# Kernel tuning notes

Hardware: AMD Instinct MI355X
Metric: run time of the kernel (lower is better)

Reference implementation:

```python
import jax, jax.numpy as jnp
import numpy as np

N = 100000

def gcn_conv(x, edge_index, W, b, num_nodes):
    # PyG GCNConv: add self-loops, symmetric deg^{-1/2} normalization, then linear.
    xw = x @ W  # [N, out]
    loops = jnp.arange(num_nodes, dtype=edge_index.dtype)
    src = jnp.concatenate([edge_index[0], loops])
    dst = jnp.concatenate([edge_index[1], loops])
    deg = jax.ops.segment_sum(jnp.ones_like(src, dtype=xw.dtype), dst, num_segments=num_nodes)
    dinv = jnp.where(deg > 0, jax.lax.rsqrt(deg), 0.0)
    norm = dinv[src] * dinv[dst]            # [E+N]
    msg = xw[src] * norm[:, None]           # gather + scale
    out = jax.ops.segment_sum(msg, dst, num_segments=num_nodes)  # scatter-add
    return out + b


def setup_inputs() -> dict:
    key = jax.random.key(0)
    ks = jax.random.split(key, 12)
    in_feat, hid, out_c = 64, 64, 16
    E = 1000000
    x = jax.random.normal(ks[0], (N, in_feat), dtype=jnp.float32)
    ei_spatial = jax.random.randint(ks[1], (2, E), 0, N, dtype=jnp.int32)
    ei_sim = jax.random.randint(ks[2], (2, E), 0, N, dtype=jnp.int32)
    def glorot(k, fi, fo):
        s = jnp.sqrt(6.0 / (fi + fo))
        return jax.random.uniform(k, (fi, fo), jnp.float32, -s, s)
    return {
        "x": x, "ei_spatial": ei_spatial, "ei_sim": ei_sim,
        "W1a": glorot(ks[3], in_feat, hid), "b1a": jnp.zeros((hid,), jnp.float32),
        "W1b": glorot(ks[4], in_feat, hid), "b1b": jnp.zeros((hid,), jnp.float32),
        "W2a": glorot(ks[5], hid, out_c), "b2a": jnp.zeros((out_c,), jnp.float32),
        "W2b": glorot(ks[6], hid, out_c), "b2b": jnp.zeros((out_c,), jnp.float32),
    }


def reference(x, ei_spatial, ei_sim, W1a, b1a, W1b, b1b, W2a, b2a, W2b, b2b):
    # HeteroConv layer 1: mean over the two relation-specific GCNConvs
    h = 0.5 * (gcn_conv(x, ei_spatial, W1a, b1a, N) + gcn_conv(x, ei_sim, W1b, b1b, N))
    h = jax.nn.relu(h)
    # HeteroConv layer 2
    out = 0.5 * (gcn_conv(h, ei_spatial, W2a, b2a, N) + gcn_conv(h, ei_sim, W2b, b2b, N))
    return out
```

## Files before the change

kernel.cpp:

```cpp
#include <hip/hip_runtime.h>

#define XS_STRIDE 72
#define MAXBUK 256
#define BF_CHUNK 4096

typedef unsigned short ushort_t;
typedef unsigned int uint_t;
typedef __attribute__((ext_vector_type(8))) short short8_t;
typedef __attribute__((ext_vector_type(4))) float f32x4;

__device__ __forceinline__ ushort_t f2bf(float x) {
    uint_t u = __float_as_uint(x);
    uint_t r = (u + 0x7FFFu + ((u >> 16) & 1u)) >> 16;
    return (ushort_t)r;
}
__device__ __forceinline__ float bf2f(ushort_t h) {
    return __uint_as_float((uint_t)h << 16);
}
__device__ __forceinline__ float bf2f_lo(uint_t g) { return __uint_as_float(g << 16); }
__device__ __forceinline__ float bf2f_hi(uint_t g) { return __uint_as_float(g & 0xFFFF0000u); }

__global__ void init_caps_kernel(int* bcursor2, int nbuk2, int CAP) {
    int i = blockIdx.x * blockDim.x + threadIdx.x;
    if (i < nbuk2) bcursor2[i] = i * CAP;
}

__global__ void bfill2_kernel(const int* __restrict__ eia, const int* __restrict__ eib,
                              int* __restrict__ bcursor, uint_t* __restrict__ pairs,
                              int Ea, int Eb, int Et, int shift, int nbuk, int n) {
    __shared__ int cnt[MAXBUK];
    __shared__ int base[MAXBUK];
    __shared__ int off[MAXBUK];
    const int t = threadIdx.x;
    const long long e0 = (long long)blockIdx.x * BF_CHUNK;
    const int nedge = (int)min((long long)BF_CHUNK, (long long)Et - e0);
    const int nbuk2 = 2 * nbuk;
    const uint_t mask = (1u << shift) - 1u;
    for (int i = t; i < nbuk2; i += 256) cnt[i] = 0;
    __syncthreads();
    for (int i = t; i < nedge; i += 256) {
        long long e = e0 + i;
        int rel = (e >= Ea);
        int d = rel ? eib[Eb + (e - Ea)] : eia[Ea + e];
        atomicAdd(&cnt[(rel ? nbuk : 0) + (d >> shift)], 1);
    }
    __syncthreads();
    for (int i = t; i < nbuk2; i += 256) {
        off[i] = 0;
        base[i] = cnt[i] ? atomicAdd(&bcursor[i], cnt[i]) : 0;
    }
    __syncthreads();
    for (int i = t; i < nedge; i += 256) {
        long long e = e0 + i;
        int rel = (e >= Ea);
        int s, d;
        if (rel) { s = eib[e - Ea]; d = eib[Eb + (e - Ea)]; }
        else     { s = eia[e];      d = eia[Ea + e]; }
        int b = (rel ? nbuk : 0) + (d >> shift);
        int p = base[b] + atomicAdd(&off[b], 1);
        pairs[p] = ((uint_t)s << shift) | ((uint_t)d & mask);
    }
}

template<int NPB>
__global__ void bucket_csr_kernel(const uint_t* __restrict__ pairs,
                                  const int* __restrict__ bcursor2,
                                  int2* __restrict__ rowse2, float* __restrict__ dinv2,
                                  int* __restrict__ col2,
                                  int nbuk, int shift, int n, int CAP) {
    constexpr int BLK = 1024;
    constexpr int K = NPB / BLK;
    constexpr uint_t MASK = NPB - 1;
    __shared__ int cnt[NPB];
    __shared__ int wsum[16];
    const int b = blockIdx.x;
    const int t = threadIdx.x;
    const int lane = t & 63;
    const int w = t >> 6;
    const int rel = (b >= nbuk);
    const int blocal = rel ? b - nbuk : b;
    const int nodelo = blocal << shift;
    const int node0 = (rel ? n : 0) + nodelo;
    const int NN = min(NPB, n - nodelo);
    const int p0 = b * CAP;
    const int p1 = bcursor2[b];

    #pragma unroll
    for (int k = 0; k < K; ++k) cnt[t + k * BLK] = 0;
    __syncthreads();
    for (int idx = p0 + t; idx < p1; idx += BLK)
        atomicAdd(&cnt[pairs[idx] & MASK], 1);
    __syncthreads();

    int a[K]; int s = 0;
    #pragma unroll
    for (int k = 0; k < K; ++k) { a[k] = cnt[t * K + k]; s += a[k]; }
    int sc = s;
    #pragma unroll
    for (int d = 1; d < 64; d <<= 1) {
        int u = __shfl_up(sc, d);
        if (lane >= d) sc += u;
    }
    if (lane == 63) wsum[w] = sc;
    __syncthreads();
    if (t < 16) {
        int v = wsum[t];
        int scc = v;
        #pragma unroll
        for (int d = 1; d < 16; d <<= 1) {
            int u = __shfl_up(scc, d);
            if (t >= d) scc += u;
        }
        wsum[t] = scc - v;
    }
    __syncthreads();
    int run = p0 + wsum[w] + sc - s;
    __syncthreads();
    #pragma unroll
    for (int k = 0; k < K; ++k) {
        int j = t * K + k;
        cnt[j] = run;
        if (j < NN) {
            rowse2[node0 + j] = make_int2(run, run + a[k]);
            dinv2[node0 + j] = rsqrtf((float)(a[k] + 1));
        }
        run += a[k];
    }
    __syncthreads();
    for (int idx = p0 + t; idx < p1; idx += BLK) {
        uint_t p = pairs[idx];
        int pos = atomicAdd(&cnt[p & MASK], 1);
        col2[pos] = (int)(p >> shift);
    }
}

__global__ void gemm2_mfma_bf16_kernel(const float* __restrict__ X,
                                       const float* __restrict__ Wa, const float* __restrict__ Wb,
                                       const float* __restrict__ dinva, const float* __restrict__ dinvb,
                                       ushort_t* __restrict__ ya, ushort_t* __restrict__ yb, int n) {
    __shared__ ushort_t Xs[64 * XS_STRIDE];
    __shared__ ushort_t Wt[128 * XS_STRIDE];
    const int tid = threadIdx.x;
    const int rowbase = blockIdx.x * 64;

    {
        int row = tid >> 2, cg = tid & 3;
        int grow = rowbase + row;
        float4 v[4];
        if (grow < n) {
            const float4* xr = reinterpret_cast<const float4*>(X + (size_t)grow * 64 + cg * 16);
            v[0] = xr[0]; v[1] = xr[1]; v[2] = xr[2]; v[3] = xr[3];
        } else {
            v[0] = v[1] = v[2] = v[3] = make_float4(0.f, 0.f, 0.f, 0.f);
        }
        ushort_t* dst = &Xs[row * XS_STRIDE + cg * 16];
        #pragma unroll
        for (int q = 0; q < 4; ++q) {
            dst[q * 4 + 0] = f2bf(v[q].x); dst[q * 4 + 1] = f2bf(v[q].y);
            dst[q * 4 + 2] = f2bf(v[q].z); dst[q * 4 + 3] = f2bf(v[q].w);
        }
    }
    for (int idx = tid; idx < 4096; idx += 256) {
        int k = idx >> 6, c = idx & 63;
        Wt[c * XS_STRIDE + k] = f2bf(Wa[idx]);
        Wt[(64 + c) * XS_STRIDE + k] = f2bf(Wb[idx]);
    }
    __syncthreads();

    const int wid = tid >> 6, lane = tid & 63;
    const int lrow = lane & 15;
    const int lk = (lane >> 4) * 8;

    short8_t a0 = *reinterpret_cast<const short8_t*>(&Xs[(wid * 16 + lrow) * XS_STRIDE + lk]);
    short8_t a1 = *reinterpret_cast<const short8_t*>(&Xs[(wid * 16 + lrow) * XS_STRIDE + 32 + lk]);

    f32x4 acc[8];
    #pragma unroll
    for (int ct = 0; ct < 8; ++ct) {
        short8_t b0 = *reinterpret_cast<const short8_t*>(&Wt[(ct * 16 + lrow) * XS_STRIDE + lk]);
        short8_t b1 = *reinterpret_cast<const short8_t*>(&Wt[(ct * 16 + lrow) * XS_STRIDE + 32 + lk]);
        f32x4 c = {0.f, 0.f, 0.f, 0.f};
        c = __builtin_amdgcn_mfma_f32_16x16x32_bf16(a0, b0, c, 0, 0, 0);
        c = __builtin_amdgcn_mfma_f32_16x16x32_bf16(a1, b1, c, 0, 0, 0);
        acc[ct] = c;
    }

    const int rq = (lane >> 4) * 4;
    #pragma unroll
    for (int r = 0; r < 4; ++r) {
        int grow = rowbase + wid * 16 + rq + r;
        if (grow < n) {
            float sa = dinva[grow], sb = dinvb[grow];
            #pragma unroll
            for (int ct = 0; ct < 8; ++ct) {
                int col = ct * 16 + lrow;
                float v = acc[ct][r];
                if (col < 64) ya[(size_t)grow * 64 + col] = f2bf(v * sa);
                else          yb[(size_t)grow * 64 + (col - 64)] = f2bf(v * sb);
            }
        }
    }
}

__global__ void gemm2_mfma_h_kernel(const ushort_t* __restrict__ H,
                                    const float* __restrict__ W2a, const float* __restrict__ W2b,
                                    const float* __restrict__ dinva, const float* __restrict__ dinvb,
                                    ushort_t* __restrict__ za, ushort_t* __restrict__ zb, int n) {
    __shared__ ushort_t Hs[64 * XS_STRIDE];
    __shared__ ushort_t Wt[32 * XS_STRIDE];
    const int tid = threadIdx.x;
    const int rowbase = blockIdx.x * 64;

    {
        int row = tid >> 2, cg = tid & 3;
        int grow = rowbase + row;
        uint4 v0 = {0, 0, 0, 0}, v1 = {0, 0, 0, 0};
        if (grow < n) {
            const uint4* hr = reinterpret_cast<const uint4*>(H + (size_t)grow * 64 + cg * 16);
            v0 = hr[0]; v1 = hr[1];
        }
        uint4* dst = reinterpret_cast<uint4*>(&Hs[row * XS_STRIDE + cg * 16]);
        dst[0] = v0; dst[1] = v1;
    }
    for (int idx = tid; idx < 2048; idx += 256) {
        int c = idx & 31, k = idx >> 5;
        float v = (c < 16) ? W2a[k * 16 + c] : W2b[k * 16 + (c - 16)];
        Wt[c * XS_STRIDE + k] = f2bf(v);
    }
    __syncthreads();

    const int wid = tid >> 6, lane = tid & 63;
    const int lrow = lane & 15;
    const int lk = (lane >> 4) * 8;
    const int rq = (lane >> 4) * 4;

    short8_t a0 = *reinterpret_cast<const short8_t*>(&Hs[(wid * 16 + lrow) * XS_STRIDE + lk]);
    short8_t a1 = *reinterpret_cast<const short8_t*>(&Hs[(wid * 16 + lrow) * XS_STRIDE + 32 + lk]);

    f32x4 c0 = {0.f, 0.f, 0.f, 0.f}, c1 = {0.f, 0.f, 0.f, 0.f};
    {
        short8_t b0 = *reinterpret_cast<const short8_t*>(&Wt[lrow * XS_STRIDE + lk]);
        short8_t b1 = *reinterpret_cast<const short8_t*>(&Wt[lrow * XS_STRIDE + 32 + lk]);
        c0 = __builtin_amdgcn_mfma_f32_16x16x32_bf16(a0, b0, c0, 0, 0, 0);
        c0 = __builtin_amdgcn_mfma_f32_16x16x32_bf16(a1, b1, c0, 0, 0, 0);
    }
    {
        short8_t b0 = *reinterpret_cast<const short8_t*>(&Wt[(16 + lrow) * XS_STRIDE + lk]);
        short8_t b1 = *reinterpret_cast<const short8_t*>(&Wt[(16 + lrow) * XS_STRIDE + 32 + lk]);
        c1 = __builtin_amdgcn_mfma_f32_16x16x32_bf16(a0, b0, c1, 0, 0, 0);
        c1 = __builtin_amdgcn_mfma_f32_16x16x32_bf16(a1, b1, c1, 0, 0, 0);
    }
    #pragma unroll
    for (int r = 0; r < 4; ++r) {
        int node = rowbase + wid * 16 + rq + r;
        if (node < n) {
            za[(size_t)node * 16 + lrow] = f2bf(c0[r] * dinva[node]);
            zb[(size_t)node * 16 + lrow] = f2bf(c1[r] * dinvb[node]);
        }
    }
}

__global__ void __launch_bounds__(256, 8)
agg64_dual_kernel(const ushort_t* __restrict__ ya, const ushort_t* __restrict__ yb,
                  const int2* __restrict__ rowse2, const int* __restrict__ col2,
                  const float* __restrict__ dinv2,
                  const float* __restrict__ ba, const float* __restrict__ bb,
                  ushort_t* __restrict__ h, int n) {
    const int lane = threadIdx.x & 63;
    const int half = lane >> 5;
    const int fp   = lane & 31;
    const int gw   = (blockIdx.x * blockDim.x + threadIdx.x) >> 6;
    const int nw   = (gridDim.x * blockDim.x) >> 6;
    const float bx = ba[2 * fp] + bb[2 * fp];
    const float by = ba[2 * fp + 1] + bb[2 * fp + 1];
    for (int i = gw; i < n; i += nw) {
        const int2 sea = rowse2[i];
        const int2 seb = rowse2[n + i];
        float ax = 0.f, ay = 0.f, bx2 = 0.f, by2 = 0.f;
        if (half == 0) {
            uint_t ga = *reinterpret_cast<const uint_t*>(ya + (size_t)i * 64 + 2 * fp);
            uint_t gb = *reinterpret_cast<const uint_t*>(yb + (size_t)i * 64 + 2 * fp);
            ax = bf2f_lo(ga); ay = bf2f_hi(ga);
            bx2 = bf2f_lo(gb); by2 = bf2f_hi(gb);
        }
        for (int base0 = sea.x; base0 < sea.y; base0 += 64) {
            const int m = min(64, sea.y - base0);
            int cv = (lane < m) ? col2[base0 + lane] : 0;
            int j = 0;
            for (; j + 8 <= m; j += 8) {
                int c0 = __shfl(cv, j + half),     c1 = __shfl(cv, j + 2 + half);
                int c2 = __shfl(cv, j + 4 + half), c3 = __shfl(cv, j + 6 + half);
                uint_t g0 = *reinterpret_cast<const uint_t*>(ya + (size_t)c0 * 64 + 2 * fp);
                uint_t g1 = *reinterpret_cast<const uint_t*>(ya + (size_t)c1 * 64 + 2 * fp);
                uint_t g2 = *reinterpret_cast<const uint_t*>(ya + (size_t)c2 * 64 + 2 * fp);
                uint_t g3 = *reinterpret_cast<const uint_t*>(ya + (size_t)c3 * 64 + 2 * fp);
                ax += (bf2f_lo(g0) + bf2f_lo(g1)) + (bf2f_lo(g2) + bf2f_lo(g3));
                ay += (bf2f_hi(g0) + bf2f_hi(g1)) + (bf2f_hi(g2) + bf2f_hi(g3));
            }
            for (; j + 2 <= m; j += 2) {
                int c = __shfl(cv, j + half);
                uint_t g = *reinterpret_cast<const uint_t*>(ya + (size_t)c * 64 + 2 * fp);
                ax += bf2f_lo(g); ay += bf2f_hi(g);
            }
            if (j < m) {
                int c = __shfl(cv, j);
                if (half == 0) {
                    uint_t g = *reinterpret_cast<const uint_t*>(ya + (size_t)c * 64 + 2 * fp);
                    ax += bf2f_lo(g); ay += bf2f_hi(g);
                }
            }
        }
        for (int base0 = seb.x; base0 < seb.y; base0 += 64) {
            const int m = min(64, seb.y - base0);
            int cv = (lane < m) ? col2[base0 + lane] : 0;
            int j = 0;
            for (; j + 8 <= m; j += 8) {
                int c0 = __shfl(cv, j + half),     c1 = __shfl(cv, j + 2 + half);
                int c2 = __shfl(cv, j + 4 + half), c3 = __shfl(cv, j + 6 + half);
                uint_t g0 = *reinterpret_cast<const uint_t*>(yb + (size_t)c0 * 64 + 2 * fp);
                uint_t g1 = *reinterpret_cast<const uint_t*>(yb + (size_t)c1 * 64 + 2 * fp);
                uint_t g2 = *reinterpret_cast<const uint_t*>(yb + (size_t)c2 * 64 + 2 * fp);
                uint_t g3 = *reinterpret_cast<const uint_t*>(yb + (size_t)c3 * 64 + 2 * fp);
                bx2 += (bf2f_lo(g0) + bf2f_lo(g1)) + (bf2f_lo(g2) + bf2f_lo(g3));
                by2 += (bf2f_hi(g0) + bf2f_hi(g1)) + (bf2f_hi(g2) + bf2f_hi(g3));
            }
            for (; j + 2 <= m; j += 2) {
                int c = __shfl(cv, j + half);
                uint_t g = *reinterpret_cast<const uint_t*>(yb + (size_t)c * 64 + 2 * fp);
                bx2 += bf2f_lo(g); by2 += bf2f_hi(g);
            }
            if (j < m) {
                int c = __shfl(cv, j);
                if (half == 0) {
                    uint_t g = *reinterpret_cast<const uint_t*>(yb + (size_t)c * 64 + 2 * fp);
                    bx2 += bf2f_lo(g); by2 += bf2f_hi(g);
                }
            }
        }
        ax += __shfl_xor(ax, 32);  ay += __shfl_xor(ay, 32);
        bx2 += __shfl_xor(bx2, 32); by2 += __shfl_xor(by2, 32);
        const float da = dinv2[i], db = dinv2[n + i];
        if (half == 0) {
            float vx = fmaxf(0.5f * (ax * da + bx2 * db + bx), 0.0f);
            float vy = fmaxf(0.5f * (ay * da + by2 * db + by), 0.0f);
            uint_t p = (uint_t)f2bf(vx) | ((uint_t)f2bf(vy) << 16);
            *reinterpret_cast<uint_t*>(h + (size_t)i * 64 + 2 * fp) = p;
        }
    }
}

__global__ void __launch_bounds__(256, 8)
agg16_dual_kernel(const ushort_t* __restrict__ za, const ushort_t* __restrict__ zb,
                  const int2* __restrict__ rowse2, const int* __restrict__ col2,
                  const float* __restrict__ dinv2,
                  const float* __restrict__ ba, const float* __restrict__ bb,
                  float* __restrict__ outp, int n) {
    const int lane = threadIdx.x & 63;
    const int fp   = lane & 7;
    const int sub  = lane >> 3;
    const int gw   = (blockIdx.x * blockDim.x + threadIdx.x) >> 6;
    const int nw   = (gridDim.x * blockDim.x) >> 6;
    const float bx = ba[2 * fp] + bb[2 * fp];
    const float by = ba[2 * fp + 1] + bb[2 * fp + 1];
    for (int i = gw; i < n; i += nw) {
        const int2 sea = rowse2[i];
        const int2 seb = rowse2[n + i];
        int ea = sea.x + sub, eb = seb.x + sub;
        const int e1a = sea.y, e1b = seb.y;
        float ax = 0.f, ay = 0.f, bx2 = 0.f, by2 = 0.f;
        if (sub == 0) {
            uint_t ga = *reinterpret_cast<const uint_t*>(za + (size_t)i * 16 + 2 * fp);
            uint_t gb = *reinterpret_cast<const uint_t*>(zb + (size_t)i * 16 + 2 * fp);
            ax = bf2f_lo(ga); ay = bf2f_hi(ga);
            bx2 = bf2f_lo(gb); by2 = bf2f_hi(gb);
        }
        for (; ea + 8 < e1a && eb + 8 < e1b; ea += 16, eb += 16) {
            int c0 = col2[ea], c1 = col2[ea + 8];
            int d0 = col2[eb], d1 = col2[eb + 8];
            uint_t g0 = *reinterpret_cast<const uint_t*>(za + (size_t)c0 * 16 + 2 * fp);
            uint_t g1 = *reinterpret_cast<const uint_t*>(za + (size_t)c1 * 16 + 2 * fp);
            uint_t g2 = *reinterpret_cast<const uint_t*>(zb + (size_t)d0 * 16 + 2 * fp);
            uint_t g3 = *reinterpret_cast<const uint_t*>(zb + (size_t)d1 * 16 + 2 * fp);
            ax += bf2f_lo(g0) + bf2f_lo(g1);  ay += bf2f_hi(g0) + bf2f_hi(g1);
            bx2 += bf2f_lo(g2) + bf2f_lo(g3); by2 += bf2f_hi(g2) + bf2f_hi(g3);
        }
        for (; ea < e1a; ea += 8) {
            uint_t g = *reinterpret_cast<const uint_t*>(za + (size_t)col2[ea] * 16 + 2 * fp);
            ax += bf2f_lo(g); ay += bf2f_hi(g);
        }
        for (; eb < e1b; eb += 8) {
            uint_t g = *reinterpret_cast<const uint_t*>(zb + (size_t)col2[eb] * 16 + 2 * fp);
            bx2 += bf2f_lo(g); by2 += bf2f_hi(g);
        }
        const float da = dinv2[i], db = dinv2[n + i];
        float vx = ax * da + bx2 * db;
        float vy = ay * da + by2 * db;
        vx += __shfl_xor(vx, 8);  vy += __shfl_xor(vy, 8);
        vx += __shfl_xor(vx, 16); vy += __shfl_xor(vy, 16);
        vx += __shfl_xor(vx, 32); vy += __shfl_xor(vy, 32);
        if (sub == 0) {
            float2 o = make_float2(0.5f * (vx + bx), 0.5f * (vy + by));
            *reinterpret_cast<float2*>(outp + (size_t)i * 16 + 2 * fp) = o;
        }
    }
}

extern "C" void kernel_launch(void* const* d_in, const int* in_sizes, int n_in,
                              void* d_out, int out_size, void* d_ws, size_t ws_size,
                              hipStream_t stream) {
    const float* x   = (const float*)d_in[0];
    const int*   eia = (const int*)d_in[1];
    const int*   eib = (const int*)d_in[2];
    const float* W1a = (const float*)d_in[3];
    const float* b1a = (const float*)d_in[4];
    const float* W1b = (const float*)d_in[5];
    const float* b1b = (const float*)d_in[6];
    const float* W2a = (const float*)d_in[7];
    const float* b2a = (const float*)d_in[8];
    const float* W2b = (const float*)d_in[9];
    const float* b2b = (const float*)d_in[10];
    float* out = (float*)d_out;

    const int n  = in_sizes[0] / 64;
    const int Ea = in_sizes[1] / 2;
    const int Eb = in_sizes[2] / 2;
    const int Et = Ea + Eb;
    const int n2 = 2 * n;

    int shift = 10;
    while ((((long long)n + (1LL << shift) - 1) >> shift) > 128) ++shift;
    const int nbuk = (int)(((long long)n + (1LL << shift) - 1) >> shift);
    const int nbuk2 = 2 * nbuk;
    const int Emaxrel = Ea > Eb ? Ea : Eb;
    int CAP = ((Emaxrel / (nbuk > 0 ? nbuk : 1)) * 3) / 2 + 2048;
    CAP = (CAP + 63) & ~63;

    char* wsp = (char*)d_ws;
    size_t off = 0;
    auto carve = [&](size_t elems) { void* p = wsp + off; off += ((elems + 3) & ~(size_t)3) * 4; return p; };
    float* dinv2    = (float*)carve(n2);
    int2*  rowse2   = (int2*)carve((size_t)n2 * 2);
    int*   bcursor2 = (int*)carve(MAXBUK);
    int*   col2     = (int*)carve((size_t)nbuk2 * CAP);
    ushort_t* ya    = (ushort_t*)carve((size_t)32 * n);
    ushort_t* yb    = (ushort_t*)carve((size_t)32 * n);
    ushort_t* za    = (ushort_t*)carve((size_t)8 * n);
    ushort_t* zb    = (ushort_t*)carve((size_t)8 * n);
    size_t pair_words = (size_t)nbuk2 * CAP;
    size_t big_words = pair_words > (size_t)32 * n ? pair_words : (size_t)32 * n;
    void*  big      = carve(big_words);
    uint_t* pairs   = (uint_t*)big;
    ushort_t* H     = (ushort_t*)big;

    const int T = 256;
    auto cdiv = [](long long a, long long b) { return (unsigned)((a + b - 1) / b); };

    init_caps_kernel<<<1, 256, 0, stream>>>(bcursor2, nbuk2, CAP);
    bfill2_kernel<<<cdiv(Et, BF_CHUNK), T, 0, stream>>>(eia, eib, bcursor2, pairs,
                                                        Ea, Eb, Et, shift, nbuk, n);
    if (shift == 10)
        bucket_csr_kernel<1024><<<nbuk2, 1024, 0, stream>>>(pairs, bcursor2, rowse2, dinv2,
                                                            col2, nbuk, shift, n, CAP);
    else if (shift == 11)
        bucket_csr_kernel<2048><<<nbuk2, 1024, 0, stream>>>(pairs, bcursor2, rowse2, dinv2,
                                                            col2, nbuk, shift, n, CAP);
    else
        bucket_csr_kernel<4096><<<nbuk2, 1024, 0, stream>>>(pairs, bcursor2, rowse2, dinv2,
                                                            col2, nbuk, shift, n, CAP);

    const unsigned AGG_GRID = 2048;

    gemm2_mfma_bf16_kernel<<<cdiv(n, 64), T, 0, stream>>>(x, W1a, W1b, dinv2, dinv2 + n, ya, yb, n);
    agg64_dual_kernel<<<AGG_GRID, T, 0, stream>>>(ya, yb, rowse2, col2, dinv2, b1a, b1b, H, n);

    gemm2_mfma_h_kernel<<<cdiv(n, 64), T, 0, stream>>>(H, W2a, W2b, dinv2, dinv2 + n, za, zb, n);
    agg16_dual_kernel<<<AGG_GRID, T, 0, stream>>>(za, zb, rowse2, col2, dinv2, b2a, b2b, out, n);
}
```

Before: 168.2 us.

## Interleave per-node CSR ranges and dinv, widen agg64 gathers to 8 bytes

Row start/end pairs for both relations are now packed as one int4 per node, and the two dinv values as one float2, so each consumer kernel does a single vector load instead of two scattered loads. The 64-feature aggregation kernel is also restructured so each lane gathers 4 bf16 features (8 bytes) while the wave handles 4 edges at once, instead of 2 features across 2 half-waves. The aim is fewer load instructions and better memory coalescing. The cost is an extra cross-lane reduction stage and more accumulator registers.

```diff
diff --git a/kernel.cpp b/kernel.cpp
--- a/kernel.cpp
+++ b/kernel.cpp
@@ -65,7 +65,7 @@
 template<int NPB>
 __global__ void bucket_csr_kernel(const uint_t* __restrict__ pairs,
                                   const int* __restrict__ bcursor2,
-                                  int2* __restrict__ rowse2, float* __restrict__ dinv2,
+                                  int* __restrict__ rowse, float* __restrict__ dinv,
                                   int* __restrict__ col2,
                                   int nbuk, int shift, int n, int CAP) {
     constexpr int BLK = 1024;
@@ -80,7 +80,6 @@
     const int rel = (b >= nbuk);
     const int blocal = rel ? b - nbuk : b;
     const int nodelo = blocal << shift;
-    const int node0 = (rel ? n : 0) + nodelo;
     const int NN = min(NPB, n - nodelo);
     const int p0 = b * CAP;
     const int p1 = bcursor2[b];
@@ -121,8 +120,10 @@
         int j = t * K + k;
         cnt[j] = run;
         if (j < NN) {
-            rowse2[node0 + j] = make_int2(run, run + a[k]);
-            dinv2[node0 + j] = rsqrtf((float)(a[k] + 1));
+            int node = nodelo + j;
+            *reinterpret_cast<int2*>(rowse + 4 * (size_t)node + (rel ? 2 : 0)) =
+                make_int2(run, run + a[k]);
+            dinv[2 * (size_t)node + rel] = rsqrtf((float)(a[k] + 1));
         }
         run += a[k];
     }
@@ -136,7 +137,7 @@
 
 __global__ void gemm2_mfma_bf16_kernel(const float* __restrict__ X,
                                        const float* __restrict__ Wa, const float* __restrict__ Wb,
-                                       const float* __restrict__ dinva, const float* __restrict__ dinvb,
+                                       const float2* __restrict__ dinv,
                                        ushort_t* __restrict__ ya, ushort_t* __restrict__ yb, int n) {
     __shared__ ushort_t Xs[64 * XS_STRIDE];
     __shared__ ushort_t Wt[128 * XS_STRIDE];
@@ -190,13 +191,13 @@
     for (int r = 0; r < 4; ++r) {
         int grow = rowbase + wid * 16 + rq + r;
         if (grow < n) {
-            float sa = dinva[grow], sb = dinvb[grow];
+            float2 dv = dinv[grow];
             #pragma unroll
             for (int ct = 0; ct < 8; ++ct) {
                 int col = ct * 16 + lrow;
                 float v = acc[ct][r];
-                if (col < 64) ya[(size_t)grow * 64 + col] = f2bf(v * sa);
-                else          yb[(size_t)grow * 64 + (col - 64)] = f2bf(v * sb);
+                if (col < 64) ya[(size_t)grow * 64 + col] = f2bf(v * dv.x);
+                else          yb[(size_t)grow * 64 + (col - 64)] = f2bf(v * dv.y);
             }
         }
     }
@@ -204,7 +205,7 @@
 
 __global__ void gemm2_mfma_h_kernel(const ushort_t* __restrict__ H,
                                     const float* __restrict__ W2a, const float* __restrict__ W2b,
-                                    const float* __restrict__ dinva, const float* __restrict__ dinvb,
+                                    const float2* __restrict__ dinv,
                                     ushort_t* __restrict__ za, ushort_t* __restrict__ zb, int n) {
     __shared__ ushort_t Hs[64 * XS_STRIDE];
     __shared__ ushort_t Wt[32 * XS_STRIDE];
@@ -254,105 +255,124 @@
     for (int r = 0; r < 4; ++r) {
         int node = rowbase + wid * 16 + rq + r;
         if (node < n) {
-            za[(size_t)node * 16 + lrow] = f2bf(c0[r] * dinva[node]);
-            zb[(size_t)node * 16 + lrow] = f2bf(c1[r] * dinvb[node]);
+            float2 dv = dinv[node];
+            za[(size_t)node * 16 + lrow] = f2bf(c0[r] * dv.x);
+            zb[(size_t)node * 16 + lrow] = f2bf(c1[r] * dv.y);
         }
     }
 }
 
 __global__ void __launch_bounds__(256, 8)
 agg64_dual_kernel(const ushort_t* __restrict__ ya, const ushort_t* __restrict__ yb,
-                  const int2* __restrict__ rowse2, const int* __restrict__ col2,
-                  const float* __restrict__ dinv2,
+                  const int4* __restrict__ rowse4, const int* __restrict__ col2,
+                  const float2* __restrict__ dinv,
                   const float* __restrict__ ba, const float* __restrict__ bb,
                   ushort_t* __restrict__ h, int n) {
     const int lane = threadIdx.x & 63;
-    const int half = lane >> 5;
-    const int fp   = lane & 31;
-    const int gw   = (blockIdx.x * blockDim.x + threadIdx.x) >> 6;
-    const int nw   = (gridDim.x * blockDim.x) >> 6;
-    const float bx = ba[2 * fp] + bb[2 * fp];
-    const float by = ba[2 * fp + 1] + bb[2 * fp + 1];
+    const int quarter = lane >> 4;
+    const int fp = lane & 15;
+    const int gw = (blockIdx.x * blockDim.x + threadIdx.x) >> 6;
+    const int nw = (gridDim.x * blockDim.x) >> 6;
+    const float bi0 = ba[4 * fp] + bb[4 * fp];
+    const float bi1 = ba[4 * fp + 1] + bb[4 * fp + 1];
+    const float bi2 = ba[4 * fp + 2] + bb[4 * fp + 2];
+    const float bi3 = ba[4 * fp + 3] + bb[4 * fp + 3];
     for (int i = gw; i < n; i += nw) {
-        const int2 sea = rowse2[i];
-        const int2 seb = rowse2[n + i];
-        float ax = 0.f, ay = 0.f, bx2 = 0.f, by2 = 0.f;
-        if (half == 0) {
-            uint_t ga = *reinterpret_cast<const uint_t*>(ya + (size_t)i * 64 + 2 * fp);
-            uint_t gb = *reinterpret_cast<const uint_t*>(yb + (size_t)i * 64 + 2 * fp);
-            ax = bf2f_lo(ga); ay = bf2f_hi(ga);
-            bx2 = bf2f_lo(gb); by2 = bf2f_hi(gb);
-        }
-        for (int base0 = sea.x; base0 < sea.y; base0 += 64) {
-            const int m = min(64, sea.y - base0);
+        const int4 se = rowse4[i];
+        const float2 dv = dinv[i];
+        float a0 = 0.f, a1 = 0.f, a2 = 0.f, a3 = 0.f;
+        float c0 = 0.f, c1 = 0.f, c2 = 0.f, c3 = 0.f;
+        if (quarter == 0) {
+            uint2 g = *reinterpret_cast<const uint2*>(ya + (size_t)i * 64 + 4 * fp);
+            a0 = bf2f_lo(g.x); a1 = bf2f_hi(g.x); a2 = bf2f_lo(g.y); a3 = bf2f_hi(g.y);
+            uint2 gb = *reinterpret_cast<const uint2*>(yb + (size_t)i * 64 + 4 * fp);
+            c0 = bf2f_lo(gb.x); c1 = bf2f_hi(gb.x); c2 = bf2f_lo(gb.y); c3 = bf2f_hi(gb.y);
+        }
+        for (int base0 = se.x; base0 < se.y; base0 += 64) {
+            const int m = min(64, se.y - base0);
             int cv = (lane < m) ? col2[base0 + lane] : 0;
             int j = 0;
             for (; j + 8 <= m; j += 8) {
-                int c0 = __shfl(cv, j + half),     c1 = __shfl(cv, j + 2 + half);
-                int c2 = __shfl(cv, j + 4 + half), c3 = __shfl(cv, j + 6 + half);
-                uint_t g0 = *reinterpret_cast<const uint_t*>(ya + (size_t)c0 * 64 + 2 * fp);
-                uint_t g1 = *reinterpret_cast<const uint_t*>(ya + (size_t)c1 * 64 + 2 * fp);
-                uint_t g2 = *reinterpret_cast<const uint_t*>(ya + (size_t)c2 * 64 + 2 * fp);
-                uint_t g3 = *reinterpret_cast<const uint_t*>(ya + (size_t)c3 * 64 + 2 * fp);
-                ax += (bf2f_lo(g0) + bf2f_lo(g1)) + (bf2f_lo(g2) + bf2f_lo(g3));
-                ay += (bf2f_hi(g0) + bf2f_hi(g1)) + (bf2f_hi(g2) + bf2f_hi(g3));
-            }
-            for (; j + 2 <= m; j += 2) {
-                int c = __shfl(cv, j + half);
-                uint_t g = *reinterpret_cast<const uint_t*>(ya + (size_t)c * 64 + 2 * fp);
-                ax += bf2f_lo(g); ay += bf2f_hi(g);
+                int e0 = __shfl(cv, j + quarter);
+                int e1 = __shfl(cv, j + 4 + quarter);
+                uint2 g0 = *reinterpret_cast<const uint2*>(ya + (size_t)e0 * 64 + 4 * fp);
+                uint2 g1 = *reinterpret_cast<const uint2*>(ya + (size_t)e1 * 64 + 4 * fp);
+                a0 += bf2f_lo(g0.x) + bf2f_lo(g1.x);
+                a1 += bf2f_hi(g0.x) + bf2f_hi(g1.x);
+                a2 += bf2f_lo(g0.y) + bf2f_lo(g1.y);
+                a3 += bf2f_hi(g0.y) + bf2f_hi(g1.y);
             }
             if (j < m) {
-                int c = __shfl(cv, j);
-                if (half == 0) {
-                    uint_t g = *reinterpret_cast<const uint_t*>(ya + (size_t)c * 64 + 2 * fp);
-                    ax += bf2f_lo(g); ay += bf2f_hi(g);
+                int i0 = j + quarter, i1 = j + 4 + quarter;
+                int e0 = __shfl(cv, i0 & 63);
+                int e1 = __shfl(cv, i1 & 63);
+                if (i0 < m) {
+                    uint2 g = *reinterpret_cast<const uint2*>(ya + (size_t)e0 * 64 + 4 * fp);
+                    a0 += bf2f_lo(g.x); a1 += bf2f_hi(g.x);
+                    a2 += bf2f_lo(g.y); a3 += bf2f_hi(g.y);
+                }
+                if (i1 < m) {
+                    uint2 g = *reinterpret_cast<const uint2*>(ya + (size_t)e1 * 64 + 4 * fp);
+                    a0 += bf2f_lo(g.x); a1 += bf2f_hi(g.x);
+                    a2 += bf2f_lo(g.y); a3 += bf2f_hi(g.y);
                 }
             }
         }
-        for (int base0 = seb.x; base0 < seb.y; base0 += 64) {
-            const int m = min(64, seb.y - base0);
+        for (int base0 = se.z; base0 < se.w; base0 += 64) {
+            const int m = min(64, se.w - base0);
             int cv = (lane < m) ? col2[base0 + lane] : 0;
             int j = 0;
             for (; j + 8 <= m; j += 8) {
-                int c0 = __shfl(cv, j + half),     c1 = __shfl(cv, j + 2 + half);
-                int c2 = __shfl(cv, j + 4 + half), c3 = __shfl(cv, j + 6 + half);
-                uint_t g0 = *reinterpret_cast<const uint_t*>(yb + (size_t)c0 * 64 + 2 * fp);
-                uint_t g1 = *reinterpret_cast<const uint_t*>(yb + (size_t)c1 * 64 + 2 * fp);
-                uint_t g2 = *reinterpret_cast<const uint_t*>(yb + (size_t)c2 * 64 + 2 * fp);
-                uint_t g3 = *reinterpret_cast<const uint_t*>(yb + (size_t)c3 * 64 + 2 * fp);
-                bx2 += (bf2f_lo(g0) + bf2f_lo(g1)) + (bf2f_lo(g2) + bf2f_lo(g3));
-                by2 += (bf2f_hi(g0) + bf2f_hi(g1)) + (bf2f_hi(g2) + bf2f_hi(g3));
-            }
-            for (; j + 2 <= m; j += 2) {
-                int c = __shfl(cv, j + half);
-                uint_t g = *reinterpret_cast<const uint_t*>(yb + (size_t)c * 64 + 2 * fp);
-                bx2 += bf2f_lo(g); by2 += bf2f_hi(g);
+                int e0 = __shfl(cv, j + quarter);
+                int e1 = __shfl(cv, j + 4 + quarter);
+                uint2 g0 = *reinterpret_cast<const uint2*>(yb + (size_t)e0 * 64 + 4 * fp);
+                uint2 g1 = *reinterpret_cast<const uint2*>(yb + (size_t)e1 * 64 + 4 * fp);
+                c0 += bf2f_lo(g0.x) + bf2f_lo(g1.x);
+                c1 += bf2f_hi(g0.x) + bf2f_hi(g1.x);
+                c2 += bf2f_lo(g0.y) + bf2f_lo(g1.y);
+                c3 += bf2f_hi(g0.y) + bf2f_hi(g1.y);
             }
             if (j < m) {
-                int c = __shfl(cv, j);
-                if (half == 0) {
-                    uint_t g = *reinterpret_cast<const uint_t*>(yb + (size_t)c * 64 + 2 * fp);
-                    bx2 += bf2f_lo(g); by2 += bf2f_hi(g);
+                int i0 = j + quarter, i1 = j + 4 + quarter;
+                int e0 = __shfl(cv, i0 & 63);
+                int e1 = __shfl(cv, i1 & 63);
+                if (i0 < m) {
+                    uint2 g = *reinterpret_cast<const uint2*>(yb + (size_t)e0 * 64 + 4 * fp);
+                    c0 += bf2f_lo(g.x); c1 += bf2f_hi(g.x);
+                    c2 += bf2f_lo(g.y); c3 += bf2f_hi(g.y);
+                }
+                if (i1 < m) {
+                    uint2 g = *reinterpret_cast<const uint2*>(yb + (size_t)e1 * 64 + 4 * fp);
+                    c0 += bf2f_lo(g.x); c1 += bf2f_hi(g.x);
+                    c2 += bf2f_lo(g.y); c3 += bf2f_hi(g.y);
                 }
             }
         }
-        ax += __shfl_xor(ax, 32);  ay += __shfl_xor(ay, 32);
-        bx2 += __shfl_xor(bx2, 32); by2 += __shfl_xor(by2, 32);
-        const float da = dinv2[i], db = dinv2[n + i];
-        if (half == 0) {
-            float vx = fmaxf(0.5f * (ax * da + bx2 * db + bx), 0.0f);
-            float vy = fmaxf(0.5f * (ay * da + by2 * db + by), 0.0f);
-            uint_t p = (uint_t)f2bf(vx) | ((uint_t)f2bf(vy) << 16);
-            *reinterpret_cast<uint_t*>(h + (size_t)i * 64 + 2 * fp) = p;
+        float v0 = a0 * dv.x + c0 * dv.y;
+        float v1 = a1 * dv.x + c1 * dv.y;
+        float v2 = a2 * dv.x + c2 * dv.y;
+        float v3 = a3 * dv.x + c3 * dv.y;
+        v0 += __shfl_xor(v0, 16); v1 += __shfl_xor(v1, 16);
+        v2 += __shfl_xor(v2, 16); v3 += __shfl_xor(v3, 16);
+        v0 += __shfl_xor(v0, 32); v1 += __shfl_xor(v1, 32);
+        v2 += __shfl_xor(v2, 32); v3 += __shfl_xor(v3, 32);
+        if (quarter == 0) {
+            float r0 = fmaxf(0.5f * (v0 + bi0), 0.0f);
+            float r1 = fmaxf(0.5f * (v1 + bi1), 0.0f);
+            float r2 = fmaxf(0.5f * (v2 + bi2), 0.0f);
+            float r3 = fmaxf(0.5f * (v3 + bi3), 0.0f);
+            uint2 p;
+            p.x = (uint_t)f2bf(r0) | ((uint_t)f2bf(r1) << 16);
+            p.y = (uint_t)f2bf(r2) | ((uint_t)f2bf(r3) << 16);
+            *reinterpret_cast<uint2*>(h + (size_t)i * 64 + 4 * fp) = p;
         }
     }
 }
 
 __global__ void __launch_bounds__(256, 8)
 agg16_dual_kernel(const ushort_t* __restrict__ za, const ushort_t* __restrict__ zb,
-                  const int2* __restrict__ rowse2, const int* __restrict__ col2,
-                  const float* __restrict__ dinv2,
+                  const int4* __restrict__ rowse4, const int* __restrict__ col2,
+                  const float2* __restrict__ dinv,
                   const float* __restrict__ ba, const float* __restrict__ bb,
                   float* __restrict__ outp, int n) {
     const int lane = threadIdx.x & 63;
@@ -363,10 +383,10 @@
     const float bx = ba[2 * fp] + bb[2 * fp];
     const float by = ba[2 * fp + 1] + bb[2 * fp + 1];
     for (int i = gw; i < n; i += nw) {
-        const int2 sea = rowse2[i];
-        const int2 seb = rowse2[n + i];
-        int ea = sea.x + sub, eb = seb.x + sub;
-        const int e1a = sea.y, e1b = seb.y;
+        const int4 se = rowse4[i];
+        const float2 dv = dinv[i];
+        int ea = se.x + sub, eb = se.z + sub;
+        const int e1a = se.y, e1b = se.w;
         float ax = 0.f, ay = 0.f, bx2 = 0.f, by2 = 0.f;
         if (sub == 0) {
             uint_t ga = *reinterpret_cast<const uint_t*>(za + (size_t)i * 16 + 2 * fp);
@@ -392,9 +412,8 @@
             uint_t g = *reinterpret_cast<const uint_t*>(zb + (size_t)col2[eb] * 16 + 2 * fp);
             bx2 += bf2f_lo(g); by2 += bf2f_hi(g);
         }
-        const float da = dinv2[i], db = dinv2[n + i];
-        float vx = ax * da + bx2 * db;
-        float vy = ay * da + by2 * db;
+        float vx = ax * dv.x + bx2 * dv.y;
+        float vy = ay * dv.x + by2 * dv.y;
         vx += __shfl_xor(vx, 8);  vy += __shfl_xor(vy, 8);
         vx += __shfl_xor(vx, 16); vy += __shfl_xor(vy, 16);
         vx += __shfl_xor(vx, 32); vy += __shfl_xor(vy, 32);
@@ -438,8 +457,8 @@
     char* wsp = (char*)d_ws;
     size_t off = 0;
     auto carve = [&](size_t elems) { void* p = wsp + off; off += ((elems + 3) & ~(size_t)3) * 4; return p; };
-    float* dinv2    = (float*)carve(n2);
-    int2*  rowse2   = (int2*)carve((size_t)n2 * 2);
+    float* dinv     = (float*)carve(n2);
+    int*   rowse    = (int*)carve((size_t)n * 4);
     int*   bcursor2 = (int*)carve(MAXBUK);
     int*   col2     = (int*)carve((size_t)nbuk2 * CAP);
     ushort_t* ya    = (ushort_t*)carve((size_t)32 * n);
@@ -459,20 +478,22 @@
     bfill2_kernel<<<cdiv(Et, BF_CHUNK), T, 0, stream>>>(eia, eib, bcursor2, pairs,
                                                         Ea, Eb, Et, shift, nbuk, n);
     if (shift == 10)
-        bucket_csr_kernel<1024><<<nbuk2, 1024, 0, stream>>>(pairs, bcursor2, rowse2, dinv2,
+        bucket_csr_kernel<1024><<<nbuk2, 1024, 0, stream>>>(pairs, bcursor2, rowse, dinv,
                                                             col2, nbuk, shift, n, CAP);
     else if (shift == 11)
-        bucket_csr_kernel<2048><<<nbuk2, 1024, 0, stream>>>(pairs, bcursor2, rowse2, dinv2,
+        bucket_csr_kernel<2048><<<nbuk2, 1024, 0, stream>>>(pairs, bcursor2, rowse, dinv,
                                                             col2, nbuk, shift, n, CAP);
     else
-        bucket_csr_kernel<4096><<<nbuk2, 1024, 0, stream>>>(pairs, bcursor2, rowse2, dinv2,
+        bucket_csr_kernel<4096><<<nbuk2, 1024, 0, stream>>>(pairs, bcursor2, rowse, dinv,
                                                             col2, nbuk, shift, n, CAP);
 
     const unsigned AGG_GRID = 2048;
 
-    gemm2_mfma_bf16_kernel<<<cdiv(n, 64), T, 0, stream>>>(x, W1a, W1b, dinv2, dinv2 + n, ya, yb, n);
-    agg64_dual_kernel<<<AGG_GRID, T, 0, stream>>>(ya, yb, rowse2, col2, dinv2, b1a, b1b, H, n);
-
-    gemm2_mfma_h_kernel<<<cdiv(n, 64), T, 0, stream>>>(H, W2a, W2b, dinv2, dinv2 + n, za, zb, n);
-    agg16_dual_kernel<<<AGG_GRID, T, 0, stream>>>(za, zb, rowse2, col2, dinv2, b2a, b2b, out, n);
-}
+    gemm2_mfma_bf16_kernel<<<cdiv(n, 64), T, 0, stream>>>(x, W1a, W1b, (const float2*)dinv, ya, yb, n);
+    agg64_dual_kernel<<<AGG_GRID, T, 0, stream>>>(ya, yb, (const int4*)rowse, col2,
+                                                  (const float2*)dinv, b1a, b1b, H, n);
+
+    gemm2_mfma_h_kernel<<<cdiv(n, 64), T, 0, stream>>>(H, W2a, W2b, (const float2*)dinv, za, zb, n);
+    agg16_dual_kernel<<<AGG_GRID, T, 0, stream>>>(za, zb, (const int4*)rowse, col2,
+                                                  (const float2*)dinv, b2a, b2b, out, n);
+}
```

Result: faster. 157.1 us (-6.7%).
